# Kernel optimization log

Hardware: AMD Instinct MI355X
Metric: run time of the kernel (lower is better)

Reference implementation:

```python
import jax, jax.numpy as jnp
import numpy as np

B, S, D, H = 4, 2048, 1024, 16
HD = D // H


def setup_inputs() -> dict:
    key = jax.random.key(0)
    ks = jax.random.split(key, 5)
    scale = 1.0 / np.sqrt(D)
    return {
        "x": jax.random.normal(ks[0], (B, S, D), dtype=jnp.float32),
        "W_q": jax.random.normal(ks[1], (D, D), dtype=jnp.float32) * scale,
        "W_k": jax.random.normal(ks[2], (D, D), dtype=jnp.float32) * scale,
        "W_v": jax.random.normal(ks[3], (D, D), dtype=jnp.float32) * scale,
        "W_o": jax.random.normal(ks[4], (D, D), dtype=jnp.float32) * scale,
    }


def reference(x, W_q, W_k, W_v, W_o):
    # Linear with weight [out, in]: y = x @ W^T
    def proj(W):
        return jnp.einsum('bsd,ed->bshf', x, W.reshape(H, HD, D).transpose(0, 1, 2).reshape(D, D)) if False else (x @ W.T).reshape(B, S, H, HD).transpose(0, 2, 1, 3)

    q = proj(W_q)  # [B, H, S, HD]
    k = proj(W_k)
    v = proj(W_v)

    scores = jnp.einsum('bhqd,bhkd->bhqk', q, k) / jnp.sqrt(jnp.float32(HD))
    causal = jnp.triu(jnp.ones((S, S), dtype=bool), k=1)  # True above diagonal -> masked
    scores = jnp.where(causal, -jnp.inf, scores)
    probs = jax.nn.softmax(scores, axis=-1)
    out = jnp.einsum('bhqk,bhkd->bhqd', probs, v)  # [B, H, S, HD]
    out = out.transpose(0, 2, 1, 3).reshape(B, S, D)
    return out @ W_o.T
```

## Files before the change

kernel.cpp:

```cpp
#include <hip/hip_runtime.h>
#include <cstdint>
#include <cstddef>

typedef unsigned short u16;
typedef __attribute__((ext_vector_type(8))) short short8;
typedef __attribute__((ext_vector_type(4))) short short4v;
typedef __attribute__((ext_vector_type(8))) unsigned short ushort8v;
typedef __attribute__((ext_vector_type(4))) unsigned short ushort4v;
typedef __attribute__((ext_vector_type(4))) unsigned int uint4v;
typedef __attribute__((ext_vector_type(4))) float f32x4;

#define QSCALE 0.18033688011112042f
#define THR_L2 11.5417f


__device__ __forceinline__ u16 f2bf(float f) {
  unsigned int u = __builtin_bit_cast(unsigned int, f);
  u += 0x7FFFu + ((u >> 16) & 1u);
  return (u16)(u >> 16);
}

__device__ __forceinline__ void async16(const void* g, void* l) {
  __builtin_amdgcn_global_load_lds(
      (const __attribute__((address_space(1))) unsigned int*)g,
      (__attribute__((address_space(3))) unsigned int*)l, 16, 0, 0);
}

__device__ __forceinline__ float fmax3(float a, float b, float c) {
  float r;
  asm("v_max3_f32 %0, %1, %2, %3" : "=v"(r) : "v"(a), "v"(b), "v"(c));
  return r;
}

__device__ __forceinline__ unsigned int cvtpk(float lo, float hi) {
  unsigned int r;
  asm("v_cvt_pk_bf16_f32 %0, %1, %2" : "=v"(r) : "v"(lo), "v"(hi));
  return r;
}


__global__ void cvt_f32_bf16(const float* __restrict__ in, u16* __restrict__ out, int n) {
  int i = (blockIdx.x * 256 + threadIdx.x) * 4;
  if (i >= n) return;
  float4 v = *(const float4*)(in + i);
  ushort4v o;
  o[0] = f2bf(v.x); o[1] = f2bf(v.y); o[2] = f2bf(v.z); o[3] = f2bf(v.w);
  *(ushort4v*)(out + i) = o;
}

__global__ void cvt_w4(const float* __restrict__ a, const float* __restrict__ b,
                       const float* __restrict__ c, const float* __restrict__ d,
                       u16* __restrict__ out) {
  const int i = (blockIdx.x * 256 + threadIdx.x) * 4;
  const float* src = (blockIdx.y == 0) ? a : (blockIdx.y == 1) ? b
                    : (blockIdx.y == 2) ? c : d;
  float4 v = *(const float4*)(src + i);
  ushort4v o;
  o[0] = f2bf(v.x); o[1] = f2bf(v.y); o[2] = f2bf(v.z); o[3] = f2bf(v.w);
  *(ushort4v*)(out + (size_t)blockIdx.y * 1048576 + i) = o;
}


template<int MODE>
__global__ __launch_bounds__(256, 2) void gemm_bt(
    const u16* __restrict__ A, const u16* __restrict__ Bw,
    void* __restrict__ Cout, int M, int N, int K)
{
  const int t = threadIdx.x;
  const int lane = t & 63, w = t >> 6;
  const int li = lane & 15, g = lane >> 4;
  const int wr = w >> 1, wc = w & 1;
  const int brow = blockIdx.y * 128, bcol = blockIdx.x * 128;

  __shared__ u16 As[128 * 32];
  __shared__ u16 Bs[128 * 32];

  f32x4 acc[4][4];
#pragma unroll
  for (int i = 0; i < 4; ++i)
#pragma unroll
    for (int j = 0; j < 4; ++j) acc[i][j] = f32x4{0.f, 0.f, 0.f, 0.f};

  for (int k0 = 0; k0 < K; k0 += 32) {
#pragma unroll
    for (int L = 0; L < 2; ++L) {
      const int f = t + 256 * L;
      const int row = f >> 2;
      const int cb = ((f & 3) * 16) ^ ((row & 3) << 4);
      async16(A + (size_t)(brow + row) * K + k0 + (cb >> 1),
              &As[(w * 64 + 256 * L) * 8]);
      async16(Bw + (size_t)(bcol + row) * K + k0 + (cb >> 1),
              &Bs[(w * 64 + 256 * L) * 8]);
    }
    __syncthreads();
    short8 af[4], bfr[4];
    const int ksw = (g * 8) ^ ((li & 3) << 3);
#pragma unroll
    for (int mt = 0; mt < 4; ++mt)
      af[mt] = *(const short8*)&As[(wr * 64 + mt * 16 + li) * 32 + ksw];
#pragma unroll
    for (int nt = 0; nt < 4; ++nt)
      bfr[nt] = *(const short8*)&Bs[(wc * 64 + nt * 16 + li) * 32 + ksw];
    __builtin_amdgcn_s_setprio(1);
#pragma unroll
    for (int mt = 0; mt < 4; ++mt)
#pragma unroll
      for (int nt = 0; nt < 4; ++nt)
        acc[mt][nt] = __builtin_amdgcn_mfma_f32_16x16x32_bf16(af[mt], bfr[nt], acc[mt][nt], 0, 0, 0);
    __builtin_amdgcn_s_setprio(0);
    __syncthreads();
  }

#pragma unroll
  for (int mt = 0; mt < 4; ++mt)
#pragma unroll
    for (int nt = 0; nt < 4; ++nt) {
      const int col = bcol + wc * 64 + nt * 16 + li;
#pragma unroll
      for (int r = 0; r < 4; ++r) {
        const int row = brow + wr * 64 + mt * 16 + g * 4 + r;
        float v = acc[mt][nt][r];
        if (MODE == 0) {
          const int which = col >> 10;
          const int c2 = col & 1023;
          if (which == 0) v *= QSCALE;
          const int b = row >> 11, s = row & 2047;
          const int h = c2 >> 6, hd = c2 & 63;
          ((u16*)Cout)[(size_t)which * 8388608 +
                       (((size_t)(b * 16 + h) * 2048) + s) * 64 + hd] = f2bf(v);
        } else {
          ((float*)Cout)[(size_t)row * N + col] = v;
        }
      }
    }
}


__global__ __launch_bounds__(256) void transpose_hd_s(
    const u16* __restrict__ V, u16* __restrict__ VT)
{
  const int sb = blockIdx.x;
  const int bh = blockIdx.y;
  __shared__ u16 tile[64 * 72];
  const int t = threadIdx.x;
  const int r = t >> 3;
  const int c8 = (t & 7) * 8;
  const size_t base = (size_t)bh * 2048 * 64;
#pragma unroll
  for (int half = 0; half < 2; ++half) {
    const int row = r + 32 * half;
    ushort8v v = *(const ushort8v*)(V + base + (size_t)(sb * 64 + row) * 64 + c8);
    *(ushort8v*)&tile[row * 72 + c8] = v;
  }
  __syncthreads();
#pragma unroll
  for (int half = 0; half < 2; ++half) {
    const int hd = r + 32 * half;
    ushort8v o;
#pragma unroll
    for (int j = 0; j < 8; ++j) o[j] = tile[(c8 + j) * 72 + hd];
    *(ushort8v*)(VT + base + (size_t)hd * 2048 + sb * 64 + c8) = o;
  }
}


__global__ __launch_bounds__(256, 4) void flash_attn2(
    const u16* __restrict__ Qp, const u16* __restrict__ Kp,
    const u16* __restrict__ VTp, u16* __restrict__ Oattn)
{
  const int n = blockIdx.x;
  const int p4 = n & 3;
  const int bh = (n >> 2) & 63;
  const int t4 = n >> 8;
  int qb;
  if (t4 == 0) qb = p4;
  else if (t4 == 1) qb = 4 + (3 - p4);
  else if (t4 == 2) qb = 8 + (p4 ^ 1);
  else qb = 12 + (p4 ^ 2);

  const int t = threadIdx.x;
  const int lane = t & 63, w = t >> 6;
  const int li = lane & 15, g = lane >> 4;

  __shared__ u16 Kl[64 * 64];
  __shared__ u16 Vl[64 * 64];

  const size_t bh_off = (size_t)bh * (2048 * 64);

  short8 qf[2][2];
  int qrow[2];
#pragma unroll
  for (int qs = 0; qs < 2; ++qs) {
    qrow[qs] = qb * 128 + qs * 64 + w * 16 + li;
    const u16* qp = Qp + bh_off + (size_t)qrow[qs] * 64 + g * 8;
    qf[qs][0] = *(const short8*)qp;
    qf[qs][1] = *(const short8*)(qp + 32);
  }

  f32x4 o_acc[2][4];
#pragma unroll
  for (int qs = 0; qs < 2; ++qs)
#pragma unroll
    for (int i = 0; i < 4; ++i) o_acc[qs][i] = f32x4{0.f, 0.f, 0.f, 0.f};
  float m_i[2] = {-1e30f, -1e30f};
  float l_i[2] = {0.f, 0.f};

  const int njb = 2 * qb + 2;
  for (int jb = 0; jb < njb; ++jb) {
#pragma unroll
    for (int L = 0; L < 2; ++L) {
      const int f = t + 256 * L;
      const int kbyte = (f * 16) ^ (((f >> 3) & 7) << 4);
      async16(Kp + bh_off + (size_t)jb * 4096 + (kbyte >> 1),
              &Kl[(w * 64 + 256 * L) * 8]);
      const int vrow = f >> 3;
      const int vb = ((f & 7) * 16) ^ ((vrow & 7) << 4);
      async16(VTp + bh_off + (size_t)vrow * 2048 + jb * 64 + (vb >> 1),
              &Vl[(w * 64 + 256 * L) * 8]);
    }
    __syncthreads();

    f32x4 s_acc[2][4];
#pragma unroll
    for (int qs = 0; qs < 2; ++qs)
#pragma unroll
      for (int jt = 0; jt < 4; ++jt) s_acc[qs][jt] = f32x4{0.f, 0.f, 0.f, 0.f};
    const int ksw = (li & 7) << 3;
    __builtin_amdgcn_s_setprio(1);
#pragma unroll
    for (int kc = 0; kc < 2; ++kc)
#pragma unroll
      for (int jt = 0; jt < 4; ++jt) {
        short8 kf = *(const short8*)&Kl[(jt * 16 + li) * 64 + ((kc * 32 + g * 8) ^ ksw)];
        s_acc[0][jt] = __builtin_amdgcn_mfma_f32_16x16x32_bf16(kf, qf[0][kc], s_acc[0][jt], 0, 0, 0);
        s_acc[1][jt] = __builtin_amdgcn_mfma_f32_16x16x32_bf16(kf, qf[1][kc], s_acc[1][jt], 0, 0, 0);
      }
    __builtin_amdgcn_s_setprio(0);

    float mx[2];
    bool need = false;
#pragma unroll
    for (int qs = 0; qs < 2; ++qs) {
      if (jb * 64 + 63 > qb * 128 + qs * 64 + w * 16) {
        const int tq = qrow[qs] - jb * 64;
#pragma unroll
        for (int jt = 0; jt < 4; ++jt)
#pragma unroll
          for (int r = 0; r < 4; ++r)
            if (jt * 16 + g * 4 + r > tq) s_acc[qs][jt][r] = -1e30f;
      }
      float t0 = fmax3(s_acc[qs][0][0], s_acc[qs][0][1], s_acc[qs][0][2]);
      float t1 = fmax3(s_acc[qs][0][3], s_acc[qs][1][0], s_acc[qs][1][1]);
      float t2 = fmax3(s_acc[qs][1][2], s_acc[qs][1][3], s_acc[qs][2][0]);
      float t3 = fmax3(s_acc[qs][2][1], s_acc[qs][2][2], s_acc[qs][2][3]);
      float t4m = fmax3(s_acc[qs][3][0], s_acc[qs][3][1], s_acc[qs][3][2]);
      float m01 = fmax3(t0, t1, s_acc[qs][3][3]);
      float m23 = fmax3(t2, t3, t4m);
      float mm = fmaxf(m01, m23);
      mm = fmaxf(mm, __shfl_xor(mm, 16));
      mm = fmaxf(mm, __shfl_xor(mm, 32));
      mx[qs] = mm;
      need = need || (mm > m_i[qs] + THR_L2);
    }

    if (__any((int)need)) {
#pragma unroll
      for (int qs = 0; qs < 2; ++qs) {
        const float mn = fmaxf(m_i[qs], mx[qs]);
        const float corr = __builtin_amdgcn_exp2f(m_i[qs] - mn);
        l_i[qs] *= corr;
#pragma unroll
        for (int dt = 0; dt < 4; ++dt) o_acc[qs][dt] *= corr;
        m_i[qs] = mn;
      }
    }

    short8 pf[2][2];
#pragma unroll
    for (int qs = 0; qs < 2; ++qs) {
      const float mi = m_i[qs];
      float ps = 0.f;
#pragma unroll
      for (int jt = 0; jt < 4; ++jt)
#pragma unroll
        for (int r = 0; r < 4; ++r) {
          float e = __builtin_amdgcn_exp2f(s_acc[qs][jt][r] - mi);
          s_acc[qs][jt][r] = e;
          ps += e;
        }
      ps += __shfl_xor(ps, 16);
      ps += __shfl_xor(ps, 32);
      l_i[qs] += ps;
#pragma unroll
      for (int kc = 0; kc < 2; ++kc) {
        uint4v u;
        u[0] = cvtpk(s_acc[qs][2 * kc][0], s_acc[qs][2 * kc][1]);
        u[1] = cvtpk(s_acc[qs][2 * kc][2], s_acc[qs][2 * kc][3]);
        u[2] = cvtpk(s_acc[qs][2 * kc + 1][0], s_acc[qs][2 * kc + 1][1]);
        u[3] = cvtpk(s_acc[qs][2 * kc + 1][2], s_acc[qs][2 * kc + 1][3]);
        pf[qs][kc] = __builtin_bit_cast(short8, u);
      }
    }

    __builtin_amdgcn_s_setprio(1);
#pragma unroll
    for (int kc = 0; kc < 2; ++kc)
#pragma unroll
      for (int dt = 0; dt < 4; ++dt) {
        const int rowb = (dt * 16 + li) * 64;
        short4v v0 = *(const short4v*)&Vl[rowb + ((kc * 32 + g * 4) ^ ksw)];
        short4v v1 = *(const short4v*)&Vl[rowb + ((kc * 32 + 16 + g * 4) ^ ksw)];
        short8 vf = __builtin_shufflevector(v0, v1, 0, 1, 2, 3, 4, 5, 6, 7);
        o_acc[0][dt] = __builtin_amdgcn_mfma_f32_16x16x32_bf16(vf, pf[0][kc], o_acc[0][dt], 0, 0, 0);
        o_acc[1][dt] = __builtin_amdgcn_mfma_f32_16x16x32_bf16(vf, pf[1][kc], o_acc[1][dt], 0, 0, 0);
      }
    __builtin_amdgcn_s_setprio(0);
    __syncthreads();
  }

  const int b = bh >> 4, h = bh & 15;
#pragma unroll
  for (int qs = 0; qs < 2; ++qs) {
    const float inv_l = 1.f / l_i[qs];
    u16* op = Oattn + ((size_t)(b * 2048 + qrow[qs])) * 1024 + h * 64;
#pragma unroll
    for (int dt = 0; dt < 4; ++dt) {
      ushort4v st;
#pragma unroll
      for (int r = 0; r < 4; ++r) st[r] = f2bf(o_acc[qs][dt][r] * inv_l);
      *(ushort4v*)(op + dt * 16 + g * 4) = st;
    }
  }
}


extern "C" void kernel_launch(void* const* d_in, const int* in_sizes, int n_in,
                              void* d_out, int out_size, void* d_ws, size_t ws_size,
                              hipStream_t stream) {
  const float* x  = (const float*)d_in[0];
  const float* Wq = (const float*)d_in[1];
  const float* Wk = (const float*)d_in[2];
  const float* Wv = (const float*)d_in[3];
  const float* Wo = (const float*)d_in[4];

  const size_t NX = 8388608;
  const size_t NW = 1048576;

  u16* xb  = (u16*)d_ws;
  u16* wqb = xb + NX;
  u16* wob = wqb + 3 * NW;
  u16* Qb  = wob + NW;
  u16* Kb  = Qb + NX;
  u16* Vb  = Kb + NX;
  u16* VTb = Vb + NX;
  u16* attnb = Vb;

  cvt_f32_bf16<<<8192, 256, 0, stream>>>(x, xb, (int)NX);
  cvt_w4<<<dim3(1024, 4), 256, 0, stream>>>(Wq, Wk, Wv, Wo, wqb);

  gemm_bt<0><<<dim3(24, 64), 256, 0, stream>>>(xb, wqb, Qb, 8192, 3072, 1024);

  transpose_hd_s<<<dim3(32, 64), 256, 0, stream>>>(Vb, VTb);
  flash_attn2<<<1024, 256, 0, stream>>>(Qb, Kb, VTb, attnb);

  gemm_bt<1><<<dim3(8, 64), 256, 0, stream>>>(attnb, wob, d_out, 8192, 1024, 1024);
}
```

Measured before the change: 187.9 us.

## Pair causal query tiles per block with triple-buffered K/V pipeline and XCD-aware remap

Each attention block now handles two complementary query tiles (pr and 15-pr), so every block runs a constant 34 K/V iterations and the causal triangle is load-balanced. The single-buffered K/V loads guarded by a full syncthreads become a three-stage async pipeline that prefetches two tiles ahead, using explicit vmcnt waits and raw barriers. Both the attention grid and the GEMM grid remap block IDs so that neighbouring tiles land on the same XCD, aiming at better L2 reuse. In exchange the kernel uses three times the LDS, drops to 2 blocks per CU in its launch bounds, launches half as many blocks, and depends on hand-written waitcnt values being correct.

Result: faster. 183.4 us (-2.4%).

```diff
diff --git a/kernel.cpp b/kernel.cpp
--- a/kernel.cpp
+++ b/kernel.cpp
@@ -70,7 +70,12 @@
   const int lane = t & 63, w = t >> 6;
   const int li = lane & 15, g = lane >> 4;
   const int wr = w >> 1, wc = w & 1;
-  const int brow = blockIdx.y * 128, bcol = blockIdx.x * 128;
+
+  const int nx = gridDim.x;
+  const int hwid = blockIdx.y * nx + blockIdx.x;
+  const int cpx = (nx * gridDim.y) >> 3;
+  const int lid = (hwid & 7) * cpx + (hwid >> 3);
+  const int brow = (lid / nx) * 128, bcol = (lid % nx) * 128;
 
   __shared__ u16 As[128 * 32];
   __shared__ u16 Bs[128 * 32];
@@ -164,38 +169,40 @@
 }
 
 
-__global__ __launch_bounds__(256, 4) void flash_attn2(
+__global__ __launch_bounds__(256, 2) void flash_attn3(
     const u16* __restrict__ Qp, const u16* __restrict__ Kp,
     const u16* __restrict__ VTp, u16* __restrict__ Oattn)
 {
-  const int n = blockIdx.x;
-  const int p4 = n & 3;
-  const int bh = (n >> 2) & 63;
-  const int t4 = n >> 8;
-  int qb;
-  if (t4 == 0) qb = p4;
-  else if (t4 == 1) qb = 4 + (3 - p4);
-  else if (t4 == 2) qb = 8 + (p4 ^ 1);
-  else qb = 12 + (p4 ^ 2);
+  const int hwid = blockIdx.x;
+  const int lid = (hwid & 7) * 64 + (hwid >> 3);
+  const int pr = lid & 7, bh = lid >> 3;
 
   const int t = threadIdx.x;
   const int lane = t & 63, w = t >> 6;
   const int li = lane & 15, g = lane >> 4;
 
-  __shared__ u16 Kl[64 * 64];
-  __shared__ u16 Vl[64 * 64];
+  __shared__ u16 Kl[3][64 * 64];
+  __shared__ u16 Vl[3][64 * 64];
 
   const size_t bh_off = (size_t)bh * (2048 * 64);
-
-  short8 qf[2][2];
-  int qrow[2];
+  const int tile0 = pr, tile1 = 15 - pr;
+  const int njb0 = 2 * tile0 + 2;
+
+  short8 qf0[2][2], qf1[2][2];
 #pragma unroll
   for (int qs = 0; qs < 2; ++qs) {
-    qrow[qs] = qb * 128 + qs * 64 + w * 16 + li;
-    const u16* qp = Qp + bh_off + (size_t)qrow[qs] * 64 + g * 8;
-    qf[qs][0] = *(const short8*)qp;
-    qf[qs][1] = *(const short8*)(qp + 32);
+    const u16* qp0 = Qp + bh_off + (size_t)(tile0 * 128 + qs * 64 + w * 16 + li) * 64 + g * 8;
+    qf0[qs][0] = *(const short8*)qp0;
+    qf0[qs][1] = *(const short8*)(qp0 + 32);
+    const u16* qp1 = Qp + bh_off + (size_t)(tile1 * 128 + qs * 64 + w * 16 + li) * 64 + g * 8;
+    qf1[qs][0] = *(const short8*)qp1;
+    qf1[qs][1] = *(const short8*)(qp1 + 32);
   }
+  short8 qc[2][2];
+#pragma unroll
+  for (int qs = 0; qs < 2; ++qs) { qc[qs][0] = qf0[qs][0]; qc[qs][1] = qf0[qs][1]; }
+
+  int qbase = tile0 * 128;
 
   f32x4 o_acc[2][4];
 #pragma unroll
@@ -205,35 +212,67 @@
   float m_i[2] = {-1e30f, -1e30f};
   float l_i[2] = {0.f, 0.f};
 
-  const int njb = 2 * qb + 2;
-  for (int jb = 0; jb < njb; ++jb) {
+  const int b = bh >> 4, h = bh & 15;
+  const int ksw = (li & 7) << 3;
+
+  auto STAGE = [&](int i, int s) {
+    const int jb = (i < njb0) ? i : (i - njb0);
 #pragma unroll
     for (int L = 0; L < 2; ++L) {
       const int f = t + 256 * L;
       const int kbyte = (f * 16) ^ (((f >> 3) & 7) << 4);
       async16(Kp + bh_off + (size_t)jb * 4096 + (kbyte >> 1),
-              &Kl[(w * 64 + 256 * L) * 8]);
+              &Kl[s][(w * 64 + 256 * L) * 8]);
       const int vrow = f >> 3;
       const int vb = ((f & 7) * 16) ^ ((vrow & 7) << 4);
       async16(VTp + bh_off + (size_t)vrow * 2048 + jb * 64 + (vb >> 1),
-              &Vl[(w * 64 + 256 * L) * 8]);
-    }
-    __syncthreads();
+              &Vl[s][(w * 64 + 256 * L) * 8]);
+    }
+  };
+
+  auto WRITEO = [&]() {
+#pragma unroll
+    for (int qs = 0; qs < 2; ++qs) {
+      const float inv_l = 1.f / l_i[qs];
+      const int qrow = qbase + qs * 64 + w * 16 + li;
+      u16* op = Oattn + ((size_t)(b * 2048 + qrow)) * 1024 + h * 64;
+#pragma unroll
+      for (int dt = 0; dt < 4; ++dt) {
+        ushort4v st;
+#pragma unroll
+        for (int r = 0; r < 4; ++r) st[r] = f2bf(o_acc[qs][dt][r] * inv_l);
+        *(ushort4v*)(op + dt * 16 + g * 4) = st;
+      }
+    }
+  };
+
+  STAGE(0, 0);
+  STAGE(1, 1);
+  asm volatile("s_waitcnt vmcnt(4)" ::: "memory");
+  __builtin_amdgcn_s_barrier();
+
+#pragma unroll 1
+  for (int i = 0; i < 34; ++i) {
+    const int s = i % 3;
+    if (i + 2 < 34) STAGE(i + 2, (i + 2) % 3);
+
+    const int jb = (i < njb0) ? i : (i - njb0);
+    const u16* __restrict__ Ks = &Kl[s][0];
+    const u16* __restrict__ Vs = &Vl[s][0];
 
     f32x4 s_acc[2][4];
 #pragma unroll
     for (int qs = 0; qs < 2; ++qs)
 #pragma unroll
       for (int jt = 0; jt < 4; ++jt) s_acc[qs][jt] = f32x4{0.f, 0.f, 0.f, 0.f};
-    const int ksw = (li & 7) << 3;
     __builtin_amdgcn_s_setprio(1);
 #pragma unroll
     for (int kc = 0; kc < 2; ++kc)
 #pragma unroll
       for (int jt = 0; jt < 4; ++jt) {
-        short8 kf = *(const short8*)&Kl[(jt * 16 + li) * 64 + ((kc * 32 + g * 8) ^ ksw)];
-        s_acc[0][jt] = __builtin_amdgcn_mfma_f32_16x16x32_bf16(kf, qf[0][kc], s_acc[0][jt], 0, 0, 0);
-        s_acc[1][jt] = __builtin_amdgcn_mfma_f32_16x16x32_bf16(kf, qf[1][kc], s_acc[1][jt], 0, 0, 0);
+        short8 kf = *(const short8*)&Ks[(jt * 16 + li) * 64 + ((kc * 32 + g * 8) ^ ksw)];
+        s_acc[0][jt] = __builtin_amdgcn_mfma_f32_16x16x32_bf16(kf, qc[0][kc], s_acc[0][jt], 0, 0, 0);
+        s_acc[1][jt] = __builtin_amdgcn_mfma_f32_16x16x32_bf16(kf, qc[1][kc], s_acc[1][jt], 0, 0, 0);
       }
     __builtin_amdgcn_s_setprio(0);
 
@@ -241,8 +280,8 @@
     bool need = false;
 #pragma unroll
     for (int qs = 0; qs < 2; ++qs) {
-      if (jb * 64 + 63 > qb * 128 + qs * 64 + w * 16) {
-        const int tq = qrow[qs] - jb * 64;
+      if (jb * 64 + 63 > qbase + qs * 64 + w * 16) {
+        const int tq = qbase + qs * 64 + w * 16 + li - jb * 64;
 #pragma unroll
         for (int jt = 0; jt < 4; ++jt)
 #pragma unroll
@@ -308,29 +347,33 @@
 #pragma unroll
       for (int dt = 0; dt < 4; ++dt) {
         const int rowb = (dt * 16 + li) * 64;
-        short4v v0 = *(const short4v*)&Vl[rowb + ((kc * 32 + g * 4) ^ ksw)];
-        short4v v1 = *(const short4v*)&Vl[rowb + ((kc * 32 + 16 + g * 4) ^ ksw)];
+        short4v v0 = *(const short4v*)&Vs[rowb + ((kc * 32 + g * 4) ^ ksw)];
+        short4v v1 = *(const short4v*)&Vs[rowb + ((kc * 32 + 16 + g * 4) ^ ksw)];
         short8 vf = __builtin_shufflevector(v0, v1, 0, 1, 2, 3, 4, 5, 6, 7);
         o_acc[0][dt] = __builtin_amdgcn_mfma_f32_16x16x32_bf16(vf, pf[0][kc], o_acc[0][dt], 0, 0, 0);
         o_acc[1][dt] = __builtin_amdgcn_mfma_f32_16x16x32_bf16(vf, pf[1][kc], o_acc[1][dt], 0, 0, 0);
       }
     __builtin_amdgcn_s_setprio(0);
-    __syncthreads();
+
+    asm volatile("s_waitcnt lgkmcnt(0)" ::: "memory");
+    if (i < 32) { asm volatile("s_waitcnt vmcnt(4)" ::: "memory"); }
+    else        { asm volatile("s_waitcnt vmcnt(0)" ::: "memory"); }
+    __builtin_amdgcn_s_barrier();
+
+    if (i == njb0 - 1) {
+      WRITEO();
+      qbase = tile1 * 128;
+#pragma unroll
+      for (int qs = 0; qs < 2; ++qs) {
+        qc[qs][0] = qf1[qs][0]; qc[qs][1] = qf1[qs][1];
+        m_i[qs] = -1e30f; l_i[qs] = 0.f;
+#pragma unroll
+        for (int dt = 0; dt < 4; ++dt) o_acc[qs][dt] = f32x4{0.f, 0.f, 0.f, 0.f};
+      }
+    }
   }
 
-  const int b = bh >> 4, h = bh & 15;
-#pragma unroll
-  for (int qs = 0; qs < 2; ++qs) {
-    const float inv_l = 1.f / l_i[qs];
-    u16* op = Oattn + ((size_t)(b * 2048 + qrow[qs])) * 1024 + h * 64;
-#pragma unroll
-    for (int dt = 0; dt < 4; ++dt) {
-      ushort4v st;
-#pragma unroll
-      for (int r = 0; r < 4; ++r) st[r] = f2bf(o_acc[qs][dt][r] * inv_l);
-      *(ushort4v*)(op + dt * 16 + g * 4) = st;
-    }
-  }
+  WRITEO();
 }
 
 
@@ -361,7 +404,7 @@
   gemm_bt<0><<<dim3(24, 64), 256, 0, stream>>>(xb, wqb, Qb, 8192, 3072, 1024);
 
   transpose_hd_s<<<dim3(32, 64), 256, 0, stream>>>(Vb, VTb);
-  flash_attn2<<<1024, 256, 0, stream>>>(Qb, Kb, VTb, attnb);
+  flash_attn3<<<512, 256, 0, stream>>>(Qb, Kb, VTb, attnb);
 
   gemm_bt<1><<<dim3(8, 64), 256, 0, stream>>>(attnb, wob, d_out, 8192, 1024, 1024);
 }
```
